# Performance work log

Measured on AMD Instinct MI355X. Metric: run time of the kernel, lower is better.

The kernel has to match this reference:

```python
import jax, jax.numpy as jnp
import numpy as np

REG_COEF = 25.0


def _reflect(points, planes):
    # points: [B,P,3], planes: [B,4] -> reflected points [B,P,3]
    normals = planes[:, 0:3] / jnp.linalg.norm(planes[:, 0:3], axis=1, keepdims=True)
    offsets = planes[:, 3]
    # signed distance of each point to the plane: [B,P]
    dist = jnp.einsum('bd,bpd->bp', normals, points) + offsets[:, None]
    return points - 2.0 * dist[..., None] * normals[:, None, :]


def _chamfer(x, y):
    # x,y: [B,P,3]; pytorch3d chamfer_distance default:
    # mean over points, mean over batch, sum of both directions (squared dists)
    x2 = jnp.sum(x * x, axis=-1)  # [B,P]
    y2 = jnp.sum(y * y, axis=-1)  # [B,P]
    # pairwise squared distances [B,P,P]
    d = x2[:, :, None] + y2[:, None, :] - 2.0 * jnp.einsum('bpd,bqd->bpq', x, y)
    d = jnp.maximum(d, 0.0)
    cham_x = jnp.mean(jnp.min(d, axis=2))  # x -> nearest in y
    cham_y = jnp.mean(jnp.min(d, axis=1))  # y -> nearest in x
    return cham_x + cham_y


def _reg_loss(planes):
    # planes: [B,H,4]
    normals = planes[:, :, :3]
    normals = normals / jnp.linalg.norm(normals, axis=2, keepdims=True)
    H = normals.shape[1]
    a = jnp.einsum('bhd,bgd->bhg', normals, normals) - jnp.eye(H, dtype=normals.dtype)
    # Frobenius norm per batch -> [B]
    return jnp.sqrt(jnp.sum(a * a, axis=(1, 2)))


def setup_inputs() -> dict:
    key = jax.random.key(0)
    k1, k2 = jax.random.split(key)
    B, H, P = 8, 3, 4096
    return {
        'predicted_planes': jax.random.normal(k1, (B, H, 4), dtype=jnp.float32),
        'sample_points': jax.random.normal(k2, (B, P, 3), dtype=jnp.float32),
        'voxel_grids': jnp.zeros((B, 32, 32, 32), dtype=jnp.float32),
        'cp_grids': jnp.zeros((B, 32, 32, 32), dtype=jnp.float32),
    }


def reference(predicted_planes, sample_points, voxel_grids, cp_grids):
    n_heads = predicted_planes.shape[1]
    reg = jnp.sum(_reg_loss(predicted_planes))
    refl = jnp.asarray(0.0, dtype=sample_points.dtype)
    for h in range(n_heads):  # small fixed head count (3)
        reflected = _reflect(sample_points, predicted_planes[:, h, :])
        refl = refl + _chamfer(sample_points, reflected)
    return refl + REG_COEF * reg
```

## Files before the change

kernel.cpp:

```cpp
#include <hip/hip_runtime.h>
#include <math.h>

#define NB 8
#define NH 3
#define NBH 24
#define NP 4096
#define BLK 256
#define RPB 128
#define ROWBLKS (NP / RPB)

typedef _Float16 half8 __attribute__((ext_vector_type(8)));
typedef float floatx16 __attribute__((ext_vector_type(16)));

#define MIN3(r, a, b) asm("v_min3_f32 %0, %0, %1, %2" : "+v"(r) : "v"(a), "v"(b))

#define MFMA16(d, a, bb, c) \
    asm("v_mfma_f32_32x32x16_f16 %0, %1, %2, %3" : "=&v"(d) : "v"(a), "v"(bb), "v"(c))

__global__ void reg_kernel(const float* __restrict__ planes, float* __restrict__ out) {
    const int l = threadIdx.x;
    float r = 0.0f;
    if (l < NB) {
        float n[NH][3];
        for (int hh = 0; hh < NH; ++hh) {
            const float* pl = planes + (l * NH + hh) * 4;
            float a0 = pl[0], a1 = pl[1], a2 = pl[2];
            float inv = 1.0f / sqrtf(a0 * a0 + a1 * a1 + a2 * a2);
            n[hh][0] = a0 * inv; n[hh][1] = a1 * inv; n[hh][2] = a2 * inv;
        }
        float fro = 0.0f;
        for (int i = 0; i < NH; ++i)
            for (int j = 0; j < NH; ++j) {
                float d = n[i][0] * n[j][0] + n[i][1] * n[j][1] + n[i][2] * n[j][2]
                          - (i == j ? 1.0f : 0.0f);
                fro += d * d;
            }
        r = 25.0f * sqrtf(fro);
    }
    for (int o = 32; o; o >>= 1) r += __shfl_down(r, o);
    if (l == 0) out[0] = r;
}

__global__ void __launch_bounds__(BLK, 2) chamfer_mfma(const float* __restrict__ pts,
                                                       const float* __restrict__ planes,
                                                       float* __restrict__ out) {
    __shared__ _Float16 qcols[NP * 4];
    __shared__ float rsqbuf[RPB];
    __shared__ float bsum[4];

    const int tid  = threadIdx.x;
    const int lane = tid & 63;
    const int wave = tid >> 6;
    const int bh   = blockIdx.y;
    const int b    = bh / NH;

    const float* pl = planes + bh * 4;
    float n0 = pl[0], n1 = pl[1], n2 = pl[2], off = pl[3];
    float inv = 1.0f / sqrtf(n0 * n0 + n1 * n1 + n2 * n2);
    n0 *= inv; n1 *= inv; n2 *= inv;

    const float* bp = pts + (size_t)b * NP * 3;
    const int h = lane >> 5;

    float total = 0.0f;

    for (int dir = 0; dir < 2; ++dir) {
        for (int i = tid; i < NP; i += BLK) {
            float y0 = bp[i * 3 + 0], y1 = bp[i * 3 + 1], y2 = bp[i * 3 + 2];
            if (!dir) { float t = 2.0f * (n0 * y0 + n1 * y1 + n2 * y2 + off); y0 -= t * n0; y1 -= t * n1; y2 -= t * n2; }
            float csq = y0 * y0 + y1 * y1 + y2 * y2;
            _Float16* q = &qcols[i * 4];
            q[0] = (_Float16)(-2.0f * y0); q[1] = (_Float16)(-2.0f * y1);
            q[2] = (_Float16)(-2.0f * y2); q[3] = (_Float16)csq;
        }

        const int rlocal = wave * 32 + (lane & 31);
        const int row = blockIdx.x * RPB + rlocal;
        half8 Aev = {0, 0, 0, 0, 0, 0, 0, 0};
        half8 Aod = {0, 0, 0, 0, 0, 0, 0, 0};
        {
            float a0 = bp[row * 3 + 0], a1 = bp[row * 3 + 1], a2 = bp[row * 3 + 2];
            if (dir) { float t = 2.0f * (n0 * a0 + n1 * a1 + n2 * a2 + off); a0 -= t * n0; a1 -= t * n1; a2 -= t * n2; }
            if (lane < 32) {
                rsqbuf[rlocal] = a0 * a0 + a1 * a1 + a2 * a2;
                Aev[0] = (_Float16)a0; Aev[1] = (_Float16)a1;
                Aev[2] = (_Float16)a2; Aev[3] = (_Float16)1.0f;
                Aod[4] = (_Float16)a0; Aod[5] = (_Float16)a1;
                Aod[6] = (_Float16)a2; Aod[7] = (_Float16)1.0f;
            }
        }
        __syncthreads();

        floatx16 crsq;
        #pragma unroll
        for (int j = 0; j < 16; ++j)
            crsq[j] = rsqbuf[wave * 32 + (j & 3) + 8 * (j >> 2) + 4 * h];

        float rm[16];
        #pragma unroll
        for (int j = 0; j < 16; ++j) rm[j] = 1e30f;

        const _Float16* bcol = &qcols[(lane & 31) * 8];
        #define LD(u) (*(const half8*)(bcol + (u) * 256))

        half8 c0 = LD(0), c1 = LD(1), c2 = LD(2), c3 = LD(3);
        floatx16 dA0, dA1, dB0, dB1;
        MFMA16(dA0, Aev, c0, crsq);  MFMA16(dA1, Aod, c0, crsq);
        MFMA16(dB0, Aev, c1, crsq);  MFMA16(dB1, Aod, c1, crsq);

        #pragma unroll 1
        for (int u = 4; u <= 60; u += 4) {
            c0 = LD(u);
            #pragma unroll
            for (int j = 0; j < 16; ++j) MIN3(rm[j], dA0[j], dA1[j]);
            MFMA16(dA0, Aev, c2, crsq);  MFMA16(dA1, Aod, c2, crsq);
            c1 = LD(u + 1);
            #pragma unroll
            for (int j = 0; j < 16; ++j) MIN3(rm[j], dB0[j], dB1[j]);
            MFMA16(dB0, Aev, c3, crsq);  MFMA16(dB1, Aod, c3, crsq);
            c2 = LD(u + 2);
            #pragma unroll
            for (int j = 0; j < 16; ++j) MIN3(rm[j], dA0[j], dA1[j]);
            MFMA16(dA0, Aev, c0, crsq);  MFMA16(dA1, Aod, c0, crsq);
            c3 = LD(u + 3);
            #pragma unroll
            for (int j = 0; j < 16; ++j) MIN3(rm[j], dB0[j], dB1[j]);
            MFMA16(dB0, Aev, c1, crsq);  MFMA16(dB1, Aod, c1, crsq);
        }
        {
            #pragma unroll
            for (int j = 0; j < 16; ++j) MIN3(rm[j], dA0[j], dA1[j]);
            MFMA16(dA0, Aev, c2, crsq);  MFMA16(dA1, Aod, c2, crsq);
            #pragma unroll
            for (int j = 0; j < 16; ++j) MIN3(rm[j], dB0[j], dB1[j]);
            MFMA16(dB0, Aev, c3, crsq);  MFMA16(dB1, Aod, c3, crsq);
            #pragma unroll
            for (int j = 0; j < 16; ++j) MIN3(rm[j], dA0[j], dA1[j]);
            #pragma unroll
            for (int j = 0; j < 16; ++j) MIN3(rm[j], dB0[j], dB1[j]);
        }
        #undef LD

        #pragma unroll
        for (int j = 0; j < 16; ++j) {
            float v = rm[j];
            v = fminf(v, __shfl_xor(v, 1));
            v = fminf(v, __shfl_xor(v, 2));
            v = fminf(v, __shfl_xor(v, 4));
            v = fminf(v, __shfl_xor(v, 8));
            v = fminf(v, __shfl_xor(v, 16));
            rm[j] = v;
        }
        float s = 0.0f;
        #pragma unroll
        for (int j = 0; j < 16; ++j) s += fmaxf(rm[j], 0.0f);
        s += __shfl_xor(s, 32);
        total += s;

        __syncthreads();
    }

    if (lane == 0) bsum[wave] = total;
    __syncthreads();
    if (tid == 0)
        atomicAdd(out, (bsum[0] + bsum[1] + bsum[2] + bsum[3]) * (1.0f / (float)(NB * NP)));
}

extern "C" void kernel_launch(void* const* d_in, const int* in_sizes, int n_in,
                              void* d_out, int out_size, void* d_ws, size_t ws_size,
                              hipStream_t stream) {
    const float* planes = (const float*)d_in[0];
    const float* pts    = (const float*)d_in[1];
    float* out          = (float*)d_out;

    reg_kernel<<<1, 64, 0, stream>>>(planes, out);

    dim3 grid(ROWBLKS, NBH);
    chamfer_mfma<<<grid, BLK, 0, stream>>>(pts, planes, out);
}
```

Before: 91.71 us.

## Drop row-norm MFMA accumulator, add it after min, raise occupancy

The per-row squared norm is no longer fed in as the MFMA accumulator. The MFMAs now accumulate from zero, and the row norm is added once after the min-reduction, which is valid because it is constant per row. This removes the 16-register crsq operand and the double-buffered four-accumulator software pipeline, and replaces them with a simple loop of one tile per iteration. That frees registers so launch bounds can go from 2 to 4 blocks per SM, trading explicit MFMA/min overlap within a wave for more waves to hide latency. The MFMA result now depends directly on the next min3, so each wave serialises more, and the fp16 rounding of the pre-min values changes slightly.

```diff
diff --git a/kernel.cpp b/kernel.cpp
--- a/kernel.cpp
+++ b/kernel.cpp
@@ -14,8 +14,8 @@
 
 #define MIN3(r, a, b) asm("v_min3_f32 %0, %0, %1, %2" : "+v"(r) : "v"(a), "v"(b))
 
-#define MFMA16(d, a, bb, c) \
-    asm("v_mfma_f32_32x32x16_f16 %0, %1, %2, %3" : "=&v"(d) : "v"(a), "v"(bb), "v"(c))
+#define MFMA16Z(d, a, bb) \
+    asm("v_mfma_f32_32x32x16_f16 %0, %1, %2, 0" : "=&v"(d) : "v"(a), "v"(bb))
 
 __global__ void reg_kernel(const float* __restrict__ planes, float* __restrict__ out) {
     const int l = threadIdx.x;
@@ -41,7 +41,7 @@
     if (l == 0) out[0] = r;
 }
 
-__global__ void __launch_bounds__(BLK, 2) chamfer_mfma(const float* __restrict__ pts,
+__global__ void __launch_bounds__(BLK, 4) chamfer_mfma(const float* __restrict__ pts,
                                                        const float* __restrict__ planes,
                                                        float* __restrict__ out) {
     __shared__ _Float16 qcols[NP * 4];
@@ -91,11 +91,6 @@
         }
         __syncthreads();
 
-        floatx16 crsq;
-        #pragma unroll
-        for (int j = 0; j < 16; ++j)
-            crsq[j] = rsqbuf[wave * 32 + (j & 3) + 8 * (j >> 2) + 4 * h];
-
         float rm[16];
         #pragma unroll
         for (int j = 0; j < 16; ++j) rm[j] = 1e30f;
@@ -103,41 +98,15 @@
         const _Float16* bcol = &qcols[(lane & 31) * 8];
         #define LD(u) (*(const half8*)(bcol + (u) * 256))
 
-        half8 c0 = LD(0), c1 = LD(1), c2 = LD(2), c3 = LD(3);
-        floatx16 dA0, dA1, dB0, dB1;
-        MFMA16(dA0, Aev, c0, crsq);  MFMA16(dA1, Aod, c0, crsq);
-        MFMA16(dB0, Aev, c1, crsq);  MFMA16(dB1, Aod, c1, crsq);
-
+        half8 cb = LD(0);
         #pragma unroll 1
-        for (int u = 4; u <= 60; u += 4) {
-            c0 = LD(u);
+        for (int u = 0; u < 64; ++u) {
+            floatx16 d0, d1;
+            MFMA16Z(d0, Aev, cb);
+            MFMA16Z(d1, Aod, cb);
+            cb = LD((u + 1) & 63);
             #pragma unroll
-            for (int j = 0; j < 16; ++j) MIN3(rm[j], dA0[j], dA1[j]);
-            MFMA16(dA0, Aev, c2, crsq);  MFMA16(dA1, Aod, c2, crsq);
-            c1 = LD(u + 1);
-            #pragma unroll
-            for (int j = 0; j < 16; ++j) MIN3(rm[j], dB0[j], dB1[j]);
-            MFMA16(dB0, Aev, c3, crsq);  MFMA16(dB1, Aod, c3, crsq);
-            c2 = LD(u + 2);
-            #pragma unroll
-            for (int j = 0; j < 16; ++j) MIN3(rm[j], dA0[j], dA1[j]);
-            MFMA16(dA0, Aev, c0, crsq);  MFMA16(dA1, Aod, c0, crsq);
-            c3 = LD(u + 3);
-            #pragma unroll
-            for (int j = 0; j < 16; ++j) MIN3(rm[j], dB0[j], dB1[j]);
-            MFMA16(dB0, Aev, c1, crsq);  MFMA16(dB1, Aod, c1, crsq);
-        }
-        {
-            #pragma unroll
-            for (int j = 0; j < 16; ++j) MIN3(rm[j], dA0[j], dA1[j]);
-            MFMA16(dA0, Aev, c2, crsq);  MFMA16(dA1, Aod, c2, crsq);
-            #pragma unroll
-            for (int j = 0; j < 16; ++j) MIN3(rm[j], dB0[j], dB1[j]);
-            MFMA16(dB0, Aev, c3, crsq);  MFMA16(dB1, Aod, c3, crsq);
-            #pragma unroll
-            for (int j = 0; j < 16; ++j) MIN3(rm[j], dA0[j], dA1[j]);
-            #pragma unroll
-            for (int j = 0; j < 16; ++j) MIN3(rm[j], dB0[j], dB1[j]);
+            for (int j = 0; j < 16; ++j) MIN3(rm[j], d0[j], d1[j]);
         }
         #undef LD
 
@@ -153,7 +122,10 @@
         }
         float s = 0.0f;
         #pragma unroll
-        for (int j = 0; j < 16; ++j) s += fmaxf(rm[j], 0.0f);
+        for (int j = 0; j < 16; ++j) {
+            const int rl = wave * 32 + (j & 3) + 8 * (j >> 2) + 4 * h;
+            s += fmaxf(rsqbuf[rl] + rm[j], 0.0f);
+        }
         s += __shfl_xor(s, 32);
         total += s;
 
```

Result: slower. 95.73 us (+4.4%).
